# Kernel tuning notes

Hardware: AMD Instinct MI355X
Metric: run time of the kernel (lower is better)

Reference implementation:

```python
import jax, jax.numpy as jnp
import numpy as np

B, T, S0, S1 = 128, 16384, 64, 64  # batch, num_tiles, sizes[0], sizes[1]


def setup_inputs() -> dict:
    key = jax.random.key(0)
    k0, k1, k2, k3, k4 = jax.random.split(key, 5)
    x = jax.random.normal(k0, (B, 1, S0), dtype=jnp.float32)
    # Conv1d(1, T*S1, kernel_size=S0) weights, squeezed over the in-channel dim.
    fan1 = 1.0 / np.sqrt(S0)
    W1 = jax.random.uniform(k1, (T * S1, S0), jnp.float32, -fan1, fan1)
    b1 = jax.random.uniform(k2, (T * S1,), jnp.float32, -fan1, fan1)
    # Conv1d(T, T, kernel_size=S1, groups=T): one (1, S1) filter per tile.
    fan2 = 1.0 / np.sqrt(S1)
    W2 = jax.random.uniform(k3, (T, S1), jnp.float32, -fan2, fan2)
    b2 = jax.random.uniform(k4, (T,), jnp.float32, -fan2, fan2)
    return {"x": x, "W1": W1, "b1": b1, "W2": W2, "b2": b2}


def reference(x, W1, b1, W2, b2):
    # Conv1d(1, T*S1, kernel=S0) on length-S0 input == GEMM -> length-1 output.
    h = jnp.einsum("bs,cs->bc", x[:, 0, :], W1) + b1        # (B, T*S1)
    h = jax.nn.relu(h).reshape(x.shape[0], T, S1)            # (B, T, S1)
    # Grouped Conv1d (groups=T, 1 ch/group, kernel=S1) == per-tile dot product.
    y = jnp.einsum("btk,tk->bt", h, W2) + b2                 # (B, T)
    return (2.0 * y)[:, :, None]                             # (B, T, 1)
```

## Files before the change

### kernel.cpp

```cpp
#include <hip/hip_runtime.h>
#include <hip/hip_bf16.h>

namespace {

constexpr int T_DIM = 16384;
constexpr int NT    = 8;

typedef __attribute__((ext_vector_type(8))) short bf16x8;
typedef __attribute__((ext_vector_type(4))) float f32x4;

__device__ inline short f2bf(float f) {
    union { __hip_bfloat16 h; short s; } u;
    u.h = __float2bfloat16(f);
    return u.s;
}

__device__ inline bf16x8 cvt8(f32x4 a, f32x4 b) {
    bf16x8 r;
    r[0] = f2bf(a[0]); r[1] = f2bf(a[1]); r[2] = f2bf(a[2]); r[3] = f2bf(a[3]);
    r[4] = f2bf(b[0]); r[5] = f2bf(b[1]); r[6] = f2bf(b[2]); r[7] = f2bf(b[3]);
    return r;
}

}

__global__ __launch_bounds__(256, 4) void fgbn_kernel(
    const float* __restrict__ x,
    const float* __restrict__ W1,
    const float* __restrict__ b1,
    const float* __restrict__ W2,
    const float* __restrict__ b2,
    float* __restrict__ out)
{
    __shared__ float tile[2][4096];

    const int tid  = threadIdx.x;
    const int lane = tid & 63;
    const int wave = tid >> 6;
    const int l15  = lane & 15;
    const int l4   = lane >> 4;
    const int t0   = blockIdx.x * NT;

    bf16x8 afrag[2][2];
    #pragma unroll
    for (int rf = 0; rf < 2; ++rf) {
        const int row = wave * 32 + rf * 16 + l15;
        #pragma unroll
        for (int ks = 0; ks < 2; ++ks) {
            const float* src = x + row * 64 + ks * 32 + l4 * 8;
            afrag[rf][ks] = cvt8(*reinterpret_cast<const f32x4*>(src),
                                 *reinterpret_cast<const f32x4*>(src + 4));
        }
    }
    const float b2lane = b2[t0 + l15];

    auto stage = [&](int buf, int t) {
        const char* w1t = (const char*)W1 + (size_t)t * 16384;
        #pragma unroll
        for (int it = 0; it < 4; ++it) {
            const int c = wave * 256 + it * 64 + lane;
            const int g = c ^ ((c >> 4) & 7);
            __builtin_amdgcn_global_load_lds(
                (const __attribute__((address_space(1))) unsigned int*)(w1t + (size_t)g * 16),
                (__attribute__((address_space(3))) unsigned int*)&tile[buf][c * 4],
                16, 0, 0);
        }
    };

    float b1v[4], w2v[4];
    #pragma unroll
    for (int nf = 0; nf < 4; ++nf) {
        b1v[nf] = b1[t0 * 64 + nf * 16 + l15];
        w2v[nf] = W2[t0 * 64 + nf * 16 + l15];
    }
    stage(0, t0);
    __syncthreads();

    f32x4 outv[2] = {{0.f,0.f,0.f,0.f},{0.f,0.f,0.f,0.f}};

    for (int ti = 0; ti < NT; ++ti) {
        const int t = t0 + ti;
        const bool more = (ti + 1 < NT);

        float b1n[4], w2n[4];
        if (more) {
            stage((ti + 1) & 1, t + 1);
            #pragma unroll
            for (int nf = 0; nf < 4; ++nf) {
                b1n[nf] = b1[(t + 1) * 64 + nf * 16 + l15];
                w2n[nf] = W2[(t + 1) * 64 + nf * 16 + l15];
            }
        }

        const float* lbuf = tile[ti & 1];
        f32x4 acc[2][4];
        #pragma unroll
        for (int rf = 0; rf < 2; ++rf)
            #pragma unroll
            for (int nf = 0; nf < 4; ++nf)
                acc[rf][nf] = (f32x4){0.f, 0.f, 0.f, 0.f};

        #pragma unroll
        for (int nf = 0; nf < 4; ++nf) {
            const int j = nf * 16 + l15;
            const int sw = j & 7;
            bf16x8 bks[2];
            #pragma unroll
            for (int ks = 0; ks < 2; ++ks) {
                const int c0 = j * 16 + ks * 8 + l4 * 2;
                bks[ks] = cvt8(*reinterpret_cast<const f32x4*>(&lbuf[(c0 ^ sw) * 4]),
                               *reinterpret_cast<const f32x4*>(&lbuf[((c0 + 1) ^ sw) * 4]));
            }
            #pragma unroll
            for (int ks = 0; ks < 2; ++ks)
                #pragma unroll
                for (int rf = 0; rf < 2; ++rf)
                    acc[rf][nf] = __builtin_amdgcn_mfma_f32_16x16x32_bf16(
                        afrag[rf][ks], bks[ks], acc[rf][nf], 0, 0, 0);
        }

        #pragma unroll
        for (int rf = 0; rf < 2; ++rf) {
            #pragma unroll
            for (int r = 0; r < 4; ++r) {
                float s = 0.f;
                #pragma unroll
                for (int nf = 0; nf < 4; ++nf) {
                    const float p = fmaxf(acc[rf][nf][r] + b1v[nf], 0.f);
                    s = fmaf(p, w2v[nf], s);
                }
                s += __shfl_xor(s, 1);
                s += __shfl_xor(s, 2);
                s += __shfl_xor(s, 4);
                s += __shfl_xor(s, 8);
                const float v = 2.f * (s + b2lane);
                outv[rf][r] = (l15 == ti) ? v : outv[rf][r];
            }
        }

        if (more) {
            #pragma unroll
            for (int nf = 0; nf < 4; ++nf) { b1v[nf] = b1n[nf]; w2v[nf] = w2n[nf]; }
        }

        __syncthreads();
    }

    if (l15 < NT) {
        #pragma unroll
        for (int rf = 0; rf < 2; ++rf)
            #pragma unroll
            for (int r = 0; r < 4; ++r) {
                const int brow = wave * 32 + rf * 16 + l4 * 4 + r;
                out[(size_t)brow * T_DIM + t0 + l15] = outv[rf][r];
            }
    }
}

extern "C" void kernel_launch(void* const* d_in, const int* in_sizes, int n_in,
                              void* d_out, int out_size, void* d_ws, size_t ws_size,
                              hipStream_t stream) {
    const float* x  = (const float*)d_in[0];
    const float* W1 = (const float*)d_in[1];
    const float* b1 = (const float*)d_in[2];
    const float* W2 = (const float*)d_in[3];
    const float* b2 = (const float*)d_in[4];
    float* out = (float*)d_out;

    dim3 grid(T_DIM / NT);
    dim3 block(256);
    hipLaunchKernelGGL(fgbn_kernel, grid, block, 0, stream,
                       x, W1, b1, W2, b2, out);
}
```

Measured before the change: 59.19 us.

## Split GEMM by output channels per wave and reduce partials through LDS

Each wave now owns 16 of the 64 hidden channels for all 128 batch rows, rather than 32 batch rows across all channels. This way each wave converts only its own slice of the staged W1 tile to bf16, instead of every wave converting the whole tile. Per-wave partial dot products are written to a double-buffered LDS array and summed across waves one iteration later. Outputs are stored as 8 contiguous floats per batch row using vector stores. The trade-offs are the extra LDS traffic, holding all eight x fragments in registers (more register pressure), and the cross-wave reduction.

Measured after the change: 144.5 us. 144% more time.

```diff
diff --git a/kernel.cpp b/kernel.cpp
--- a/kernel.cpp
+++ b/kernel.cpp
@@ -33,6 +33,7 @@
     float* __restrict__ out)
 {
     __shared__ float tile[2][4096];
+    __shared__ float part[2][4][128];
 
     const int tid  = threadIdx.x;
     const int lane = tid & 63;
@@ -41,18 +42,16 @@
     const int l4   = lane >> 4;
     const int t0   = blockIdx.x * NT;
 
-    bf16x8 afrag[2][2];
+    bf16x8 xb[8][2];
     #pragma unroll
-    for (int rf = 0; rf < 2; ++rf) {
-        const int row = wave * 32 + rf * 16 + l15;
+    for (int bf = 0; bf < 8; ++bf) {
         #pragma unroll
         for (int ks = 0; ks < 2; ++ks) {
-            const float* src = x + row * 64 + ks * 32 + l4 * 8;
-            afrag[rf][ks] = cvt8(*reinterpret_cast<const f32x4*>(src),
-                                 *reinterpret_cast<const f32x4*>(src + 4));
+            const float* src = x + (bf * 16 + l15) * 64 + ks * 32 + l4 * 8;
+            xb[bf][ks] = cvt8(*reinterpret_cast<const f32x4*>(src),
+                              *reinterpret_cast<const f32x4*>(src + 4));
         }
     }
-    const float b2lane = b2[t0 + l15];
 
     auto stage = [&](int buf, int t) {
         const char* w1t = (const char*)W1 + (size_t)t * 16384;
@@ -67,93 +66,74 @@
         }
     };
 
-    float b1v[4], w2v[4];
-    #pragma unroll
-    for (int nf = 0; nf < 4; ++nf) {
-        b1v[nf] = b1[t0 * 64 + nf * 16 + l15];
-        w2v[nf] = W2[t0 * 64 + nf * 16 + l15];
-    }
+    f32x4 b1q = *reinterpret_cast<const f32x4*>(b1 + t0 * 64 + wave * 16 + l4 * 4);
+    f32x4 w2q = *reinterpret_cast<const f32x4*>(W2 + t0 * 64 + wave * 16 + l4 * 4);
+
     stage(0, t0);
     __syncthreads();
 
-    f32x4 outv[2] = {{0.f,0.f,0.f,0.f},{0.f,0.f,0.f,0.f}};
+    float yreg[NT];
 
+    #pragma unroll
     for (int ti = 0; ti < NT; ++ti) {
         const int t = t0 + ti;
         const bool more = (ti + 1 < NT);
 
-        float b1n[4], w2n[4];
+        f32x4 b1n, w2n;
         if (more) {
             stage((ti + 1) & 1, t + 1);
-            #pragma unroll
-            for (int nf = 0; nf < 4; ++nf) {
-                b1n[nf] = b1[(t + 1) * 64 + nf * 16 + l15];
-                w2n[nf] = W2[(t + 1) * 64 + nf * 16 + l15];
-            }
+            b1n = *reinterpret_cast<const f32x4*>(b1 + (t + 1) * 64 + wave * 16 + l4 * 4);
+            w2n = *reinterpret_cast<const f32x4*>(W2 + (t + 1) * 64 + wave * 16 + l4 * 4);
+        }
+
+        if (ti > 0 && tid < 128) {
+            const int p = (ti - 1) & 1;
+            const float v = part[p][0][tid] + part[p][1][tid] +
+                            part[p][2][tid] + part[p][3][tid];
+            yreg[ti - 1] = 2.f * (v + b2[t - 1]);
         }
 
         const float* lbuf = tile[ti & 1];
-        f32x4 acc[2][4];
+        const int j  = wave * 16 + l15;
+        const int sw = j & 7;
+        bf16x8 a[2];
         #pragma unroll
-        for (int rf = 0; rf < 2; ++rf)
-            #pragma unroll
-            for (int nf = 0; nf < 4; ++nf)
-                acc[rf][nf] = (f32x4){0.f, 0.f, 0.f, 0.f};
-
-        #pragma unroll
-        for (int nf = 0; nf < 4; ++nf) {
-            const int j = nf * 16 + l15;
-            const int sw = j & 7;
-            bf16x8 bks[2];
-            #pragma unroll
-            for (int ks = 0; ks < 2; ++ks) {
-                const int c0 = j * 16 + ks * 8 + l4 * 2;
-                bks[ks] = cvt8(*reinterpret_cast<const f32x4*>(&lbuf[(c0 ^ sw) * 4]),
-                               *reinterpret_cast<const f32x4*>(&lbuf[((c0 + 1) ^ sw) * 4]));
-            }
-            #pragma unroll
-            for (int ks = 0; ks < 2; ++ks)
-                #pragma unroll
-                for (int rf = 0; rf < 2; ++rf)
-                    acc[rf][nf] = __builtin_amdgcn_mfma_f32_16x16x32_bf16(
-                        afrag[rf][ks], bks[ks], acc[rf][nf], 0, 0, 0);
+        for (int ks = 0; ks < 2; ++ks) {
+            const int c0 = j * 16 + ks * 8 + l4 * 2;
+            a[ks] = cvt8(*reinterpret_cast<const f32x4*>(&lbuf[(c0 ^ sw) * 4]),
+                         *reinterpret_cast<const f32x4*>(&lbuf[((c0 + 1) ^ sw) * 4]));
         }
 
         #pragma unroll
-        for (int rf = 0; rf < 2; ++rf) {
+        for (int bf = 0; bf < 8; ++bf) {
+            f32x4 acc = (f32x4){0.f, 0.f, 0.f, 0.f};
+            acc = __builtin_amdgcn_mfma_f32_16x16x32_bf16(a[0], xb[bf][0], acc, 0, 0, 0);
+            acc = __builtin_amdgcn_mfma_f32_16x16x32_bf16(a[1], xb[bf][1], acc, 0, 0, 0);
+            float s = 0.f;
             #pragma unroll
             for (int r = 0; r < 4; ++r) {
-                float s = 0.f;
-                #pragma unroll
-                for (int nf = 0; nf < 4; ++nf) {
-                    const float p = fmaxf(acc[rf][nf][r] + b1v[nf], 0.f);
-                    s = fmaf(p, w2v[nf], s);
-                }
-                s += __shfl_xor(s, 1);
-                s += __shfl_xor(s, 2);
-                s += __shfl_xor(s, 4);
-                s += __shfl_xor(s, 8);
-                const float v = 2.f * (s + b2lane);
-                outv[rf][r] = (l15 == ti) ? v : outv[rf][r];
+                const float p = fmaxf(acc[r] + b1q[r], 0.f);
+                s = fmaf(p, w2q[r], s);
             }
+            s += __shfl_xor(s, 16);
+            s += __shfl_xor(s, 32);
+            if (l4 == 0) part[ti & 1][wave][bf * 16 + l15] = s;
         }
 
-        if (more) {
-            #pragma unroll
-            for (int nf = 0; nf < 4; ++nf) { b1v[nf] = b1n[nf]; w2v[nf] = w2n[nf]; }
-        }
+        if (more) { b1q = b1n; w2q = w2n; }
 
         __syncthreads();
     }
 
-    if (l15 < NT) {
-        #pragma unroll
-        for (int rf = 0; rf < 2; ++rf)
-            #pragma unroll
-            for (int r = 0; r < 4; ++r) {
-                const int brow = wave * 32 + rf * 16 + l4 * 4 + r;
-                out[(size_t)brow * T_DIM + t0 + l15] = outv[rf][r];
-            }
+    if (tid < 128) {
+        const int p = (NT - 1) & 1;
+        const float v = part[p][0][tid] + part[p][1][tid] +
+                        part[p][2][tid] + part[p][3][tid];
+        yreg[NT - 1] = 2.f * (v + b2[t0 + NT - 1]);
+
+        float* dst = out + (size_t)tid * T_DIM + t0;
+        *reinterpret_cast<f32x4*>(dst)     = (f32x4){yreg[0], yreg[1], yreg[2], yreg[3]};
+        *reinterpret_cast<f32x4*>(dst + 4) = (f32x4){yreg[4], yreg[5], yreg[6], yreg[7]};
     }
 }
 
```
